# Kernel tuning notes

Hardware: AMD Instinct MI355X
Metric: run time of the kernel (lower is better)

## Reference

```python
import jax, jax.numpy as jnp
import numpy as np

FRAME_LENGTH = 64   # hop size (init default)
GAIN = 0.01         # attenuate_gain


def setup_inputs() -> dict:
    key = jax.random.key(0)
    k1, k2 = jax.random.split(key)
    B, F, L = 32, 4000, 65
    noise_filter = jax.random.uniform(k1, (B, F, L), dtype=jnp.float32)
    noise = jax.random.uniform(k2, (B, F, FRAME_LENGTH), dtype=jnp.float32)
    return {"noise_filter": noise_filter, "noise": noise}


def reference(noise_filter, noise):
    B, F, L = noise_filter.shape
    hop = FRAME_LENGTH
    N = 2 * L - 1                       # odd-length zero-phase IR
    K = hop + 2 * L - 2                 # FFT-conv output length per frame
    # periodic Hann window (torch.hann_window default)
    win = 0.5 * (1.0 - jnp.cos(2.0 * jnp.pi * jnp.arange(N, dtype=jnp.float32) / N))
    # zero-phase IR from real (zero-imag) frequency response, then make linear phase
    ir = jnp.fft.irfft(noise_filter, n=N, axis=-1)          # [B,F,N]
    ir = jnp.roll(ir, L - 1, axis=-1) * win                 # windowed linear-phase IR
    H = jnp.fft.rfft(jnp.pad(ir, ((0, 0), (0, 0), (0, hop - 1))), axis=-1)   # [B,F,K//2+1]
    n = noise * 2.0 - 1.0                                   # uniform [-1,1)
    Nspec = jnp.fft.rfft(jnp.pad(n, ((0, 0), (0, 0), (0, 2 * L - 2))), axis=-1)
    frames = jnp.fft.irfft(Nspec * H, n=K, axis=-1) * GAIN  # [B,F,K]
    # overlap-add with stride = hop
    out_len = (F - 1) * hop + K
    idx = (jnp.arange(F)[:, None] * hop + jnp.arange(K)[None, :]).reshape(-1)
    out = jnp.zeros((B, out_len), frames.dtype).at[:, idx].add(frames.reshape(B, -1))
    return out
```

## Files before the change

### kernel.cpp

```cpp
#include <hip/hip_runtime.h>
#include <hip/hip_fp16.h>
#include <math.h>

#define B_    32
#define F_    4000
#define L_    65
#define N_    129
#define HOP_  64
#define K_    192
#define GF_   8
#define WAVES_ 4
#define OUTLEN_ ((F_-1)*HOP_ + K_)
#define GAIN_ 0.01f
#define BLKS_PER_B_ (F_/(GF_*WAVES_))
#define CPH_  260


__global__ __launch_bounds__(256, 2) void filtered_noise_kernel(
    const float* __restrict__ nfilt,
    const float* __restrict__ noise,
    float* __restrict__ out)
{
    __shared__ float costab[N_];
    __shared__ __half hbuf[WAVES_][2][CPH_];

    const int tid  = threadIdx.x;
    const int lane = tid & 63;
    const int wid  = __builtin_amdgcn_readfirstlane(tid >> 6);

    for (int i = tid; i < N_; i += 256)
        costab[i] = (float)cos((double)i * (2.0 * M_PI / 129.0));

    __half* hb = &hbuf[wid][0][0];
    for (int i = lane; i < 2 * CPH_; i += 64) hb[i] = __float2half(0.0f);

    __syncthreads();

    const int b  = blockIdx.x / BLKS_PER_B_;
    const int g  = (blockIdx.x % BLKS_PER_B_) * WAVES_ + wid;
    const int f0 = g * GF_;

    const int   t     = lane + 1;
    const float scale = 2.0f / 129.0f;
    const float cA = 0.5f * (1.0f - costab[64 - t]) * scale;
    const float cB = 0.5f * (1.0f - costab[64 + t]) * scale;
    const float c0 = 0.5f * (1.0f - costab[64]) * scale;

    const float c1 = costab[t];
    const float tc = 2.0f * c1;
    float sdA[4], sdB[4];
    sdA[0] = 1.0f;                 sdB[0] = c1;
    sdA[1] = costab[(16*t) % N_];  sdB[1] = costab[(17*t) % N_];
    sdA[2] = costab[(32*t) % N_];  sdB[2] = costab[(33*t) % N_];
    sdA[3] = costab[(48*t) % N_];  sdB[3] = costab[(49*t) % N_];

    const float* Xf = nfilt + (size_t)(b * F_ + f0) * L_;
    const float* Zf = noise + (size_t)(b * F_ + f0) * HOP_ + lane;
    float*       op = out + (size_t)b * OUTLEN_ + (size_t)f0 * HOP_ + lane;

    __half* hE = &hbuf[wid][0][0];
    __half* hO = &hbuf[wid][1][0];

    const int soff = (lane & 1) ? 0 : 1;
    const __half* cpsel = (lane & 1) ? hE : hO;
    const __half2* bmin = (const __half2*)cpsel + (((lane + soff + 63) >> 1) - 31);

    float wa[2] = {0,0}, wb[2] = {0,0}, wc[2] = {0,0};

    #pragma unroll 1
    for (int i = 0; i < GF_; ++i) {
        float zc = Zf[0];
        zc = fmaf(2.0f, zc, -1.0f);

        float x0 = Xf[0];
        float a = 0.5f * x0;
        float s = 0.5f * x0;
        #pragma unroll
        for (int c = 0; c < 4; ++c) {
            float ckm1 = sdA[c], ck = sdB[c];
            float aa = 0.0f, ss = 0.0f;
            #pragma unroll
            for (int q = 0; q < 16; ++q) {
                float x = Xf[c * 16 + q + 1];
                aa = fmaf(x, ck, aa);
                ss += x;
                float cn = fmaf(tc, ck, -ckm1);
                ckm1 = ck; ck = cn;
            }
            a += aa; s += ss;
        }

        __builtin_amdgcn_sched_barrier(0);
        {
            __half hA = __float2half(cA * a);
            __half hB = __float2half(cB * a);
            hE[127 - lane] = hA;  hE[129 + lane] = hB;
            hO[128 - lane] = hA;  hO[130 + lane] = hB;
            if (lane == 0) {
                __half hC = __float2half(c0 * s);
                hE[128] = hC;  hO[129] = hC;
            }
        }
        __builtin_amdgcn_sched_barrier(0);

        #pragma unroll
        for (int p = 0; p < 32; ++p) {
            const int pc = p & 1;
            float z0 = __uint_as_float(
                __builtin_amdgcn_readlane(__float_as_uint(zc), 2 * p));
            float z1 = __uint_as_float(
                __builtin_amdgcn_readlane(__float_as_uint(zc), 2 * p + 1));
            __half2 v0 = bmin[(31 - p)];
            __half2 v1 = bmin[(31 - p) + 32];
            __half2 v2 = bmin[(31 - p) + 64];
            wa[pc] = fmaf(__high2float(v0), z0, wa[pc]);
            wa[pc] = fmaf(__low2float(v0),  z1, wa[pc]);
            wb[pc] = fmaf(__high2float(v1), z0, wb[pc]);
            wb[pc] = fmaf(__low2float(v1),  z1, wb[pc]);
            wc[pc] = fmaf(__high2float(v2), z0, wc[pc]);
            wc[pc] = fmaf(__low2float(v2),  z1, wc[pc]);
        }
        __builtin_amdgcn_sched_barrier(0);

        float va = (wa[0] + wa[1]) * GAIN_;
        if (i < 2) atomicAdd(op, va); else *op = va;
        op += HOP_;
        wa[0] = wb[0]; wa[1] = wb[1];
        wb[0] = wc[0]; wb[1] = wc[1];
        wc[0] = 0.0f;  wc[1] = 0.0f;
        Xf += L_; Zf += HOP_;
    }
    atomicAdd(op,        (wa[0] + wa[1]) * GAIN_);
    atomicAdd(op + HOP_, (wb[0] + wb[1]) * GAIN_);
}

extern "C" void kernel_launch(void* const* d_in, const int* in_sizes, int n_in,
                              void* d_out, int out_size, void* d_ws, size_t ws_size,
                              hipStream_t stream) {
    const float* nfilt = (const float*)d_in[0];
    const float* noise = (const float*)d_in[1];
    float* out = (float*)d_out;

    hipMemsetAsync(d_out, 0, (size_t)out_size * sizeof(float), stream);

    dim3 grid(B_ * BLKS_PER_B_);
    dim3 block(256);
    filtered_noise_kernel<<<grid, block, 0, stream>>>(nfilt, noise, out);
}
```

Before: 213.5 us.

## Use packed fp32 FMA for IR cosine sums and fp16 dot2 for convolution

Rewrites the per-frame inverse-DFT cosine recurrence as two interleaved packed-float2 Chebyshev recurrences with step 2, so that packed FMAs halve the instruction count. Packs the noise samples to fp16 pairs via ds_bpermute and uses v_dot2 (fdot2) in the convolution loop, which replaces two readlanes and two FMAs with one readlane and one dot per pair. Raises the launch-bounds occupancy hint from 2 to 3. Rounding the noise to fp16 and the longer-stride recurrence add numerical error.

```diff
diff --git a/kernel.cpp b/kernel.cpp
--- a/kernel.cpp
+++ b/kernel.cpp
@@ -16,7 +16,27 @@
 #define CPH_  260
 
 
-__global__ __launch_bounds__(256, 2) void filtered_noise_kernel(
+typedef float    v2f __attribute__((ext_vector_type(2)));
+typedef _Float16 h2f __attribute__((ext_vector_type(2)));
+
+static __device__ __forceinline__ v2f pk_fma(v2f a, v2f b, v2f c) {
+#if __has_builtin(__builtin_elementwise_fma)
+    return __builtin_elementwise_fma(a, b, c);
+#else
+    return a * b + c;
+#endif
+}
+
+#if __has_builtin(__builtin_amdgcn_fdot2)
+#define FDOT2(a, b, c) __builtin_amdgcn_fdot2((a), (b), (c), false)
+#else
+static __device__ __forceinline__ float fdot2_sw(h2f a, h2f b, float c) {
+    return fmaf((float)a.x, (float)b.x, fmaf((float)a.y, (float)b.y, c));
+}
+#define FDOT2(a, b, c) fdot2_sw((a), (b), (c))
+#endif
+
+__global__ __launch_bounds__(256, 3) void filtered_noise_kernel(
     const float* __restrict__ nfilt,
     const float* __restrict__ noise,
     float* __restrict__ out)
@@ -46,13 +66,11 @@
     const float cB = 0.5f * (1.0f - costab[64 + t]) * scale;
     const float c0 = 0.5f * (1.0f - costab[64]) * scale;
 
-    const float c1 = costab[t];
-    const float tc = 2.0f * c1;
-    float sdA[4], sdB[4];
-    sdA[0] = 1.0f;                 sdB[0] = c1;
-    sdA[1] = costab[(16*t) % N_];  sdB[1] = costab[(17*t) % N_];
-    sdA[2] = costab[(32*t) % N_];  sdB[2] = costab[(33*t) % N_];
-    sdA[3] = costab[(48*t) % N_];  sdB[3] = costab[(49*t) % N_];
+    const float c1t = costab[t];
+    const float c2t = costab[(2 * t) % N_];
+    const float tc2 = 2.0f * c2t;
+    const v2f sck1  = {costab[(33 * t) % N_], costab[(34 * t) % N_]};
+    const v2f sckm1 = {costab[(31 * t) % N_], costab[(32 * t) % N_]};
 
     const float* Xf = nfilt + (size_t)(b * F_ + f0) * L_;
     const float* Zf = noise + (size_t)(b * F_ + f0) * HOP_ + lane;
@@ -63,7 +81,7 @@
 
     const int soff = (lane & 1) ? 0 : 1;
     const __half* cpsel = (lane & 1) ? hE : hO;
-    const __half2* bmin = (const __half2*)cpsel + (((lane + soff + 63) >> 1) - 31);
+    const h2f* bmin = (const h2f*)cpsel + (((lane + soff + 63) >> 1) - 31);
 
     float wa[2] = {0,0}, wb[2] = {0,0}, wc[2] = {0,0};
 
@@ -72,23 +90,39 @@
         float zc = Zf[0];
         zc = fmaf(2.0f, zc, -1.0f);
 
-        float x0 = Xf[0];
-        float a = 0.5f * x0;
-        float s = 0.5f * x0;
+        v2f aa0 = {0.0f, 0.0f}, aa1 = {0.0f, 0.0f}, ssv = {0.0f, 0.0f};
+        v2f ck0 = {c1t, c2t};
+        v2f km0 = {c1t, 1.0f};
+        v2f ck1 = sck1;
+        v2f km1 = sckm1;
+        const v2f tcv = {tc2, tc2};
         #pragma unroll
-        for (int c = 0; c < 4; ++c) {
-            float ckm1 = sdA[c], ck = sdB[c];
-            float aa = 0.0f, ss = 0.0f;
-            #pragma unroll
-            for (int q = 0; q < 16; ++q) {
-                float x = Xf[c * 16 + q + 1];
-                aa = fmaf(x, ck, aa);
-                ss += x;
-                float cn = fmaf(tc, ck, -ckm1);
-                ckm1 = ck; ck = cn;
-            }
-            a += aa; s += ss;
+        for (int q = 0; q < 16; ++q) {
+            v2f x0 = { Xf[2*q + 1],  Xf[2*q + 2]  };
+            v2f x1 = { Xf[2*q + 33], Xf[2*q + 34] };
+            aa0 = pk_fma(x0, ck0, aa0);
+            aa1 = pk_fma(x1, ck1, aa1);
+            ssv = ssv + x0 + x1;
+            v2f n0 = pk_fma(tcv, ck0, -km0);
+            v2f n1 = pk_fma(tcv, ck1, -km1);
+            km0 = ck0; ck0 = n0;
+            km1 = ck1; ck1 = n1;
         }
+        float x0s = Xf[0];
+        float a = 0.5f * x0s + (aa0.x + aa0.y) + (aa1.x + aa1.y);
+        float s = 0.5f * x0s + (ssv.x + ssv.y);
+
+        int za = __builtin_amdgcn_ds_bpermute(((2 * lane) & 63) << 2,
+                                              __float_as_int(zc));
+        int zb = __builtin_amdgcn_ds_bpermute(((2 * lane + 1) & 63) << 2,
+                                              __float_as_int(zc));
+#if __has_builtin(__builtin_amdgcn_cvt_pkrtz)
+        h2f vz = __builtin_bit_cast(h2f,
+            __builtin_amdgcn_cvt_pkrtz(__int_as_float(zb), __int_as_float(za)));
+#else
+        h2f vz; vz.x = (_Float16)__int_as_float(zb); vz.y = (_Float16)__int_as_float(za);
+#endif
+        const int vzi = __builtin_bit_cast(int, vz);
 
         __builtin_amdgcn_sched_barrier(0);
         {
@@ -106,19 +140,14 @@
         #pragma unroll
         for (int p = 0; p < 32; ++p) {
             const int pc = p & 1;
-            float z0 = __uint_as_float(
-                __builtin_amdgcn_readlane(__float_as_uint(zc), 2 * p));
-            float z1 = __uint_as_float(
-                __builtin_amdgcn_readlane(__float_as_uint(zc), 2 * p + 1));
-            __half2 v0 = bmin[(31 - p)];
-            __half2 v1 = bmin[(31 - p) + 32];
-            __half2 v2 = bmin[(31 - p) + 64];
-            wa[pc] = fmaf(__high2float(v0), z0, wa[pc]);
-            wa[pc] = fmaf(__low2float(v0),  z1, wa[pc]);
-            wb[pc] = fmaf(__high2float(v1), z0, wb[pc]);
-            wb[pc] = fmaf(__low2float(v1),  z1, wb[pc]);
-            wc[pc] = fmaf(__high2float(v2), z0, wc[pc]);
-            wc[pc] = fmaf(__low2float(v2),  z1, wc[pc]);
+            int zs = __builtin_amdgcn_readlane(vzi, p);
+            h2f z2 = __builtin_bit_cast(h2f, zs);
+            h2f v0 = bmin[(31 - p)];
+            h2f v1 = bmin[(31 - p) + 32];
+            h2f v2 = bmin[(31 - p) + 64];
+            wa[pc] = FDOT2(v0, z2, wa[pc]);
+            wb[pc] = FDOT2(v1, z2, wb[pc]);
+            wc[pc] = FDOT2(v2, z2, wc[pc]);
         }
         __builtin_amdgcn_sched_barrier(0);
 
```

Measured after the change: 192.3 us. 9.9% less time.
